# Kernel tuning notes

Hardware: AMD Instinct MI355X
Metric: run time of the kernel (lower is better)

Reference implementation:

```python
import jax, jax.numpy as jnp
import numpy as np
from jax import lax
from jax.scipy.special import ndtr

EV = 6           # even context kernel size
K = 3            # num_mixtures
GROUPS = 3       # grouped 1x1 convs (grps=3 for clrchs<3)
SCALE_MIN = 0.11 # lower bound on mixture std
LP = 257         # 257 CDF sampling points (8-bit Y/RGB path)


def _cdf_pts():
    # cdf_sampling_pts__Y_RGB from __init__
    pts = jnp.linspace(-127.5, 128.5, LP) / 255.0
    pts = pts.at[0].set(-147.5 / 255.0).at[-1].set(148.5 / 255.0)
    return pts.astype(jnp.float32)


def _conv(x, w, b, groups=1):
    y = lax.conv_general_dilated(
        x, w, window_strides=(1, 1), padding='VALID',
        dimension_numbers=('NCHW', 'OIHW', 'NCHW'),
        feature_group_count=groups)
    return y + b[None, :, None, None]


def _forward_float(y_condition, W0, b0, W1, b1, W2, b2):
    # replicate pad: paddd0_00_11 = (Ev//2-1, Ev//2, Ev//2-1, Ev//2)
    y = jnp.pad(y_condition, ((0, 0), (0, 0), (EV // 2 - 1, EV // 2), (EV // 2 - 1, EV // 2)), mode='edge')
    h = jax.nn.relu(_conv(y, W0, b0, groups=1))        # [B, 192, H, W]
    h = jax.nn.relu(_conv(h, W1, b1, groups=GROUPS))   # [B, 192, H, W]
    p = _conv(h, W2, b2, groups=GROUPS)                # [B, 9, H, W] GMM params
    B, _, H, W = p.shape
    p = p.reshape(B, 3, K, H, W)                       # param-major: mu / raw_scale / raw_weight
    mu, sr, wr = p[:, 0], p[:, 1], p[:, 2]             # each [B, K, H, W]
    scale = jnp.maximum(jnp.exp(sr), SCALE_MIN)
    wts = jax.nn.softmax(wr, axis=1)                   # mixture weights over K
    t = _cdf_pts()                                     # [LP]
    z = (t - mu[..., None]) / scale[..., None]         # [B, K, H, W, LP]
    cdf = jnp.einsum('bkhw,bkhwl->bhwl', wts, ndtr(z)) # mixture CDF, [B, H, W, LP]
    return jnp.clip(cdf, 0.0, 1.0 - 1e-6)


def setup_inputs() -> dict:
    key = jax.random.key(0)
    ks = jax.random.split(key, 4)
    return {
        'y_condition': jax.random.uniform(ks[0], (1, 1, 256, 256), jnp.float32),
        'W0': jax.random.normal(ks[1], (192, 1, EV, EV), jnp.float32) * 0.05,
        'b0': jnp.zeros((192,), jnp.float32),
        'W1': jax.random.normal(ks[2], (192, 64, 1, 1), jnp.float32) * 0.05,
        'b1': jnp.zeros((192,), jnp.float32),
        'W2': jax.random.normal(ks[3], (9, 64, 1, 1), jnp.float32) * 0.05,
        'b2': jnp.zeros((9,), jnp.float32),
    }


def reference(y_condition, W0, b0, W1, b1, W2, b2):
    cdf_f = _forward_float(y_condition, W0, b0, W1, b1, W2, b2)
    # _convert_to_int_and_normalize with needs_normalization=True
    new_max = jnp.float32(2 ** 16 - (LP - 1))
    cdf_i = jnp.round(cdf_f * new_max).astype(jnp.int16)
    cdf_i = cdf_i + jnp.arange(LP, dtype=jnp.int16)
    return cdf_i
```

## Files before the change

### kernel.cpp

```cpp
#include <hip/hip_runtime.h>
#include <math.h>

#define LPTS 257
#define NPIX 65536
#define PPB  32


__device__ __forceinline__ float xla_exp32(float x)
{
#pragma clang fp contract(off)
    x = fminf(x, 88.3762626647950f);
    x = fmaxf(x, -87.3365478515625f);
    const float m = floorf(fmaf(x, 1.44269504088896341f, 0.5f));
    float r = fmaf(m, -0.693359375f, x);
    r = fmaf(m, 2.12194440e-4f, r);
    const float r2 = r * r;
    float p = 1.9875691500e-4f;
    p = fmaf(p, r, 1.3981999507e-3f);
    p = fmaf(p, r, 8.3334519073e-3f);
    p = fmaf(p, r, 4.1665795894e-2f);
    p = fmaf(p, r, 1.6666665459e-1f);
    p = fmaf(p, r, 5.0000001201e-1f);
    float y = fmaf(p, r2, r) + 1.0f;
    const int e = (int)m;
    const float s = __int_as_float((e + 127) << 23);
    return y * s;
}

__device__ __forceinline__ float ieee_div(float n, float d)
{
    const float r0 = __builtin_amdgcn_rcpf(d);
    const float e  = fmaf(-d, r0, 1.0f);
    const float r1 = fmaf(e, r0, r0);
    const float q0 = n * r1;
    const float e1 = fmaf(-d, q0, n);
    const float q1 = fmaf(e1, r1, q0);
    const float e2 = fmaf(-d, q1, n);
    return fmaf(e2, r1, q1);
}

__device__ __forceinline__ float xla_erf32(float x)
{
#pragma clang fp contract(off)
    x = fminf(fmaxf(x, -4.0f), 4.0f);
    const float x2 = x * x;
    float pa = -2.72614225801306e-10f;
    pa = fmaf(pa, x2, 2.77068142495902e-08f);
    pa = fmaf(pa, x2, -2.10102402082508e-06f);
    pa = fmaf(pa, x2, -5.69250639462346e-05f);
    pa = fmaf(pa, x2, -7.34990630326855e-04f);
    pa = fmaf(pa, x2, -2.95459980854025e-03f);
    pa = fmaf(pa, x2, -1.60960333262415e-02f);
    float pb = -1.45660718464996e-05f;
    pb = fmaf(pb, x2, -2.13374055278905e-04f);
    pb = fmaf(pb, x2, -1.68282697438203e-03f);
    pb = fmaf(pb, x2, -7.37332916720468e-03f);
    pb = fmaf(pb, x2, -1.42647390514189e-02f);
    return ieee_div(x * pa, pb);
}

__device__ __forceinline__ float xla_erfc_ge1(float x)
{
#pragma clang fp contract(off)
    const float z = xla_exp32(-(x * x));
    const float q = 1.0f / x;
    const float y2 = q * q;
    float p;
    if (x < 2.0f) {
        p = 2.326819970068386e-02f;
        p = fmaf(p, y2, -1.387039388740657e-01f);
        p = fmaf(p, y2, 3.687424674597105e-01f);
        p = fmaf(p, y2, -5.824733027278666e-01f);
        p = fmaf(p, y2, 6.210004621745983e-01f);
        p = fmaf(p, y2, -4.944515323274145e-01f);
        p = fmaf(p, y2, 3.404879937665872e-01f);
        p = fmaf(p, y2, -2.741127028184656e-01f);
        p = fmaf(p, y2, 5.638259427386472e-01f);
    } else {
        p = -1.047766399936249e+01f;
        p = fmaf(p, y2, 1.297719955372516e+01f);
        p = fmaf(p, y2, -7.495518717768503e+00f);
        p = fmaf(p, y2, 2.921019019210786e+00f);
        p = fmaf(p, y2, -1.015265279202700e+00f);
        p = fmaf(p, y2, 4.218463358204948e-01f);
        p = fmaf(p, y2, -2.820767439740514e-01f);
        p = fmaf(p, y2, 5.641895067754075e-01f);
    }
    return z * q * p;
}

__device__ __forceinline__ void xla_ndtr3_y(
    float z0, float z1, float z2, float& o0, float& o1, float& o2)
{
#pragma clang fp contract(off)
    const float c = __uint_as_float(0x3f3504f3u);
    const float w0 = z0 * c, w1 = z1 * c, w2 = z2 * c;
    const float a0 = fabsf(w0), a1 = fabsf(w1), a2 = fabsf(w2);

    const float E0 = xla_erf32(w0);
    const float E1 = xla_erf32(w1);
    const float E2 = xla_erf32(w2);

    const float m0 = 1.0f - fabsf(E0);
    const float m1 = 1.0f - fabsf(E1);
    const float m2 = 1.0f - fabsf(E2);

    float y0 = (a0 < c) ? (1.0f + E0) : ((w0 > 0.0f) ? (2.0f - m0) : m0);
    float y1 = (a1 < c) ? (1.0f + E1) : ((w1 > 0.0f) ? (2.0f - m1) : m1);
    float y2 = (a2 < c) ? (1.0f + E2) : ((w2 > 0.0f) ? (2.0f - m2) : m2);

    const float amax = fmaxf(fmaxf(a0, a1), a2);
    if (__builtin_expect(__ballot(amax > 1.0f) != 0ull, 0)) {
        {
            const float ec = xla_erfc_ge1(a0);
            const float yc = (w0 > 0.0f) ? (2.0f - ec) : ec;
            y0 = (a0 > 1.0f) ? yc : y0;
        }
        {
            const float ec = xla_erfc_ge1(a1);
            const float yc = (w1 > 0.0f) ? (2.0f - ec) : ec;
            y1 = (a1 > 1.0f) ? yc : y1;
        }
        {
            const float ec = xla_erfc_ge1(a2);
            const float yc = (w2 > 0.0f) ? (2.0f - ec) : ec;
            y2 = (a2 > 1.0f) ? yc : y2;
        }
    }
    o0 = y0; o1 = y1; o2 = y2;
}

__device__ __forceinline__ float xla_ndtr32(float zf)
{
#pragma clang fp contract(off)
    const float c = __uint_as_float(0x3f3504f3u);
    const float w = zf * c;
    const float aw = fabsf(w);
    const float E = xla_erf32(w);
    const float e_mid = 1.0f - fabsf(E);
    float y = (aw < c) ? (1.0f + E)
                       : ((w > 0.0f) ? (2.0f - e_mid) : e_mid);
    if (__builtin_expect(__ballot(aw > 1.0f) != 0ull, 0)) {
        const float ec = xla_erfc_ge1(aw);
        const float yc = (w > 0.0f) ? (2.0f - ec) : ec;
        y = (aw > 1.0f) ? yc : y;
    }
    return 0.5f * y;
}

__device__ __forceinline__ int quantize(float cdf, int l)
{
    int r = (int)rintf(cdf * 65280.0f);
    r = r > 32767 ? 32767 : r;
    r = r < -32768 ? -32768 : r;
    return (int)((short)(r + l));
}

__global__ __launch_bounds__(256, 2) void entropy_params(
    const float* __restrict__ y,
    const float* __restrict__ W0, const float* __restrict__ b0,
    const float* __restrict__ W1, const float* __restrict__ b1,
    const float* __restrict__ W2, const float* __restrict__ b2,
    float* __restrict__ prm_g)
{
#pragma clang fp contract(off)
    __shared__ float tile[21][22];
    __shared__ __align__(16) float w0s[64 * 36];
    __shared__ __align__(16) float w1s[64 * 64];
    __shared__ __align__(16) float w2s[3 * 64];
    __shared__ __align__(16) float b0s[64];
    __shared__ __align__(16) float b1s[64];
    __shared__ float b2s[3];

    const int bx  = blockIdx.x & 15;
    const int by  = blockIdx.x >> 4;
    const int g   = blockIdx.y;
    const int tid = threadIdx.x;
    const int tx  = tid & 15;
    const int ty  = tid >> 4;

    {
        const float4* src = (const float4*)(W0 + g * 64 * 36);
        for (int i = tid; i < 576; i += 256) ((float4*)w0s)[i] = src[i];
    }
    {
        const float4* src = (const float4*)(W1 + g * 64 * 64);
        for (int i = tid; i < 1024; i += 256) ((float4*)w1s)[i] = src[i];
    }
    {
        const float4* src = (const float4*)(W2 + g * 3 * 64);
        if (tid < 48) ((float4*)w2s)[tid] = src[tid];
    }
    {
        const float4* s0 = (const float4*)(b0 + g * 64);
        const float4* s1 = (const float4*)(b1 + g * 64);
        if (tid < 16)      ((float4*)b0s)[tid]      = s0[tid];
        else if (tid < 32) ((float4*)b1s)[tid - 16] = s1[tid - 16];
        if (tid < 3) b2s[tid] = b2[3 * g + tid];
    }

    for (int idx = tid; idx < 21 * 21; idx += 256) {
        const int r = idx / 21;
        const int c = idx - r * 21;
        int gy = by * 16 - 2 + r; gy = gy < 0 ? 0 : (gy > 255 ? 255 : gy);
        int gx = bx * 16 - 2 + c; gx = gx < 0 ? 0 : (gx > 255 ? 255 : gx);
        tile[r][c] = y[gy * 256 + gx];
    }
    __syncthreads();

    float patch[36];
#pragma unroll
    for (int i = 0; i < 6; ++i)
#pragma unroll
        for (int j = 0; j < 6; ++j)
            patch[i * 6 + j] = tile[ty + i][tx + j];

    float h0[64];
#pragma unroll
    for (int c = 0; c < 64; ++c) {
        const float4* w4 = (const float4*)(w0s + c * 36);
        float acc = 0.0f;
#pragma unroll
        for (int q = 0; q < 9; ++q) {
            const float4 wv = w4[q];
            acc = fmaf(wv.x, patch[4 * q + 0], acc);
            acc = fmaf(wv.y, patch[4 * q + 1], acc);
            acc = fmaf(wv.z, patch[4 * q + 2], acc);
            acc = fmaf(wv.w, patch[4 * q + 3], acc);
        }
        acc = acc + b0s[c];
        h0[c] = fmaxf(acc, 0.0f);
    }

    float p0 = 0.0f, p1 = 0.0f, p2 = 0.0f;
#pragma unroll 4
    for (int c = 0; c < 64; ++c) {
        const float4* w4 = (const float4*)(w1s + c * 64);
        float acc = 0.0f;
#pragma unroll
        for (int q = 0; q < 16; ++q) {
            const float4 wv = w4[q];
            acc = fmaf(wv.x, h0[4 * q + 0], acc);
            acc = fmaf(wv.y, h0[4 * q + 1], acc);
            acc = fmaf(wv.z, h0[4 * q + 2], acc);
            acc = fmaf(wv.w, h0[4 * q + 3], acc);
        }
        acc = acc + b1s[c];
        acc = fmaxf(acc, 0.0f);
        p0 = fmaf(w2s[0 * 64 + c], acc, p0);
        p1 = fmaf(w2s[1 * 64 + c], acc, p1);
        p2 = fmaf(w2s[2 * 64 + c], acc, p2);
    }
    p0 = p0 + b2s[0];
    p1 = p1 + b2s[1];
    p2 = p2 + b2s[2];

    const int pix = (by * 16 + ty) * 256 + bx * 16 + tx;

    if (g == 0) {
        prm_g[0 * NPIX + pix] = p0;
        prm_g[1 * NPIX + pix] = p1;
        prm_g[2 * NPIX + pix] = p2;
    } else if (g == 1) {
        const float s0 = fmaxf(xla_exp32(p0), 0.11f);
        const float s1 = fmaxf(xla_exp32(p1), 0.11f);
        const float s2 = fmaxf(xla_exp32(p2), 0.11f);
        prm_g[3 * NPIX + pix] = s0;
        prm_g[4 * NPIX + pix] = s1;
        prm_g[5 * NPIX + pix] = s2;
        prm_g[6 * NPIX + pix] = 1.0f / s0;
        prm_g[7 * NPIX + pix] = 1.0f / s1;
        prm_g[8 * NPIX + pix] = 1.0f / s2;
    } else {
        const float m  = fmaxf(fmaxf(p0, p1), p2);
        const float e0 = xla_exp32(p0 - m);
        const float e1 = xla_exp32(p1 - m);
        const float e2 = xla_exp32(p2 - m);
        const float s  = (e0 + e1) + e2;
        prm_g[ 9 * NPIX + pix] = 0.5f * (e0 / s);
        prm_g[10 * NPIX + pix] = 0.5f * (e1 / s);
        prm_g[11 * NPIX + pix] = 0.5f * (e2 / s);
    }
}

__global__ __launch_bounds__(256) void entropy_cdf(
    const float* __restrict__ prm_g,
    int* __restrict__ out)
{
#pragma clang fp contract(off)
    __shared__ __align__(16) float prm[PPB][12];

    const int base = blockIdx.x * PPB;
    const int tid  = threadIdx.x;

    for (int i = tid; i < 12 * PPB; i += 256) {
        const int j = i >> 5;
        const int p = i & 31;
        prm[p][j] = prm_g[j * NPIX + base + p];
    }
    __syncthreads();

    const float CLIP = (float)(1.0 - 1e-6);

    {
        const int l = tid;
        const float t32 = (l == 0)
            ? (float)(-147.5 / 255.0)
            : (float)((((double)l) - 127.5) / 255.0);
#pragma unroll 4
        for (int p = 0; p < PPB; ++p) {
            const float4 v0 = *(const float4*)&prm[p][0];
            const float4 v1 = *(const float4*)&prm[p][4];
            const float4 v2 = *(const float4*)&prm[p][8];

            const float x0 = t32 - v0.x;
            const float x1 = t32 - v0.y;
            const float x2 = t32 - v0.z;
            const float qa = x0 * v1.z;
            const float qb = x1 * v1.w;
            const float qc = x2 * v2.x;
            const float ra = fmaf(-v0.w, qa, x0);
            const float rb = fmaf(-v1.x, qb, x1);
            const float rc = fmaf(-v1.y, qc, x2);
            const float z0 = fmaf(ra, v1.z, qa);
            const float z1 = fmaf(rb, v1.w, qb);
            const float z2 = fmaf(rc, v2.x, qc);

            float y0, y1, y2;
            xla_ndtr3_y(z0, z1, z2, y0, y1, y2);

            float cdf = fmaf(v2.w, y2, fmaf(v2.z, y1, v2.y * y0));
            cdf = fminf(fmaxf(cdf, 0.0f), CLIP);

            out[(size_t)(base + p) * LPTS + l] = quantize(cdf, l);
        }
    }

    if (tid < PPB) {
        const int p = tid;
        const float t32 = (float)(148.5 / 255.0);
        const float4 v0 = *(const float4*)&prm[p][0];
        const float4 v1 = *(const float4*)&prm[p][4];
        const float4 v2 = *(const float4*)&prm[p][8];

        const float x0 = t32 - v0.x;
        const float x1 = t32 - v0.y;
        const float x2 = t32 - v0.z;
        const float qa = x0 * v1.z;
        const float qb = x1 * v1.w;
        const float qc = x2 * v2.x;
        const float ra = fmaf(-v0.w, qa, x0);
        const float rb = fmaf(-v1.x, qb, x1);
        const float rc = fmaf(-v1.y, qc, x2);
        const float z0 = fmaf(ra, v1.z, qa);
        const float z1 = fmaf(rb, v1.w, qb);
        const float z2 = fmaf(rc, v2.x, qc);

        float y0, y1, y2;
        xla_ndtr3_y(z0, z1, z2, y0, y1, y2);

        float cdf = fmaf(v2.w, y2, fmaf(v2.z, y1, v2.y * y0));
        cdf = fminf(fmaxf(cdf, 0.0f), CLIP);

        out[(size_t)(base + p) * LPTS + 256] = quantize(cdf, 256);
    }
}

__global__ __launch_bounds__(256) void entropy_fused(
    const float* __restrict__ y,
    const float* __restrict__ W0, const float* __restrict__ b0,
    const float* __restrict__ W1, const float* __restrict__ b1,
    const float* __restrict__ W2, const float* __restrict__ b2,
    int* __restrict__ out)
{
#pragma clang fp contract(off)

    __shared__ float tile[21][22];
    __shared__ float prm[9][257];

    const int bx  = blockIdx.x & 15;
    const int by  = blockIdx.x >> 4;
    const int tid = threadIdx.x;
    const int tx  = tid & 15;
    const int ty  = tid >> 4;

    for (int idx = tid; idx < 21 * 21; idx += 256) {
        const int r = idx / 21;
        const int c = idx - r * 21;
        int gy = by * 16 - 2 + r; gy = gy < 0 ? 0 : (gy > 255 ? 255 : gy);
        int gx = bx * 16 - 2 + c; gx = gx < 0 ? 0 : (gx > 255 ? 255 : gx);
        tile[r][c] = y[gy * 256 + gx];
    }
    __syncthreads();

    float patch[36];
#pragma unroll
    for (int i = 0; i < 6; ++i)
#pragma unroll
        for (int j = 0; j < 6; ++j)
            patch[i * 6 + j] = tile[ty + i][tx + j];

    for (int g = 0; g < 3; ++g) {
        float h0[64];
#pragma unroll
        for (int c = 0; c < 64; ++c) {
            float acc = 0.0f;
            const float* w = W0 + (g * 64 + c) * 36;
#pragma unroll
            for (int k = 0; k < 36; ++k)
                acc = fmaf(w[k], patch[k], acc);
            acc = acc + b0[g * 64 + c];
            h0[c] = fmaxf(acc, 0.0f);
        }

        float p0 = 0.0f, p1 = 0.0f, p2 = 0.0f;
#pragma unroll 2
        for (int c = 0; c < 64; ++c) {
            float acc = 0.0f;
            const float* w = W1 + (g * 64 + c) * 64;
#pragma unroll
            for (int j = 0; j < 64; ++j)
                acc = fmaf(w[j], h0[j], acc);
            acc = acc + b1[g * 64 + c];
            acc = fmaxf(acc, 0.0f);
            p0 = fmaf(W2[(3 * g + 0) * 64 + c], acc, p0);
            p1 = fmaf(W2[(3 * g + 1) * 64 + c], acc, p1);
            p2 = fmaf(W2[(3 * g + 2) * 64 + c], acc, p2);
        }
        p0 = p0 + b2[3 * g + 0];
        p1 = p1 + b2[3 * g + 1];
        p2 = p2 + b2[3 * g + 2];

        if (g == 0) {
            prm[0][tid] = p0; prm[1][tid] = p1; prm[2][tid] = p2;
        } else if (g == 1) {
            prm[3][tid] = fmaxf(xla_exp32(p0), 0.11f);
            prm[4][tid] = fmaxf(xla_exp32(p1), 0.11f);
            prm[5][tid] = fmaxf(xla_exp32(p2), 0.11f);
        } else {
            const float m  = fmaxf(fmaxf(p0, p1), p2);
            const float e0 = xla_exp32(p0 - m);
            const float e1 = xla_exp32(p1 - m);
            const float e2 = xla_exp32(p2 - m);
            const float s  = (e0 + e1) + e2;
            prm[6][tid] = e0 / s;
            prm[7][tid] = e1 / s;
            prm[8][tid] = e2 / s;
        }
    }
    __syncthreads();

    const int rowbase = (by * 16) * 256 + bx * 16;
    const float CLIP = (float)(1.0 - 1e-6);

    {
        const int l = tid;
        const float t32 = (l == 0)
            ? (float)(-147.5 / 255.0)
            : (float)((((double)l) - 127.5) / 255.0);
        for (int p = 0; p < 256; ++p) {
            const float mu0 = prm[0][p], mu1 = prm[1][p], mu2 = prm[2][p];
            const float sc0 = prm[3][p], sc1 = prm[4][p], sc2 = prm[5][p];
            const float w0  = prm[6][p], w1  = prm[7][p], w2  = prm[8][p];

            const float n0 = xla_ndtr32((t32 - mu0) / sc0);
            const float n1 = xla_ndtr32((t32 - mu1) / sc1);
            const float n2 = xla_ndtr32((t32 - mu2) / sc2);

            float cdf = fmaf(w2, n2, fmaf(w1, n1, w0 * n0));
            cdf = fminf(fmaxf(cdf, 0.0f), CLIP);

            const int pix = rowbase + (p >> 4) * 256 + (p & 15);
            out[(size_t)pix * LPTS + l] = quantize(cdf, l);
        }
    }

    {
        const int p = tid;
        const float t32 = (float)(148.5 / 255.0);
        const float mu0 = prm[0][p], mu1 = prm[1][p], mu2 = prm[2][p];
        const float sc0 = prm[3][p], sc1 = prm[4][p], sc2 = prm[5][p];
        const float w0  = prm[6][p], w1  = prm[7][p], w2  = prm[8][p];

        const float n0 = xla_ndtr32((t32 - mu0) / sc0);
        const float n1 = xla_ndtr32((t32 - mu1) / sc1);
        const float n2 = xla_ndtr32((t32 - mu2) / sc2);

        float cdf = fmaf(w2, n2, fmaf(w1, n1, w0 * n0));
        cdf = fminf(fmaxf(cdf, 0.0f), CLIP);

        const int pix = rowbase + (p >> 4) * 256 + (p & 15);
        out[(size_t)pix * LPTS + 256] = quantize(cdf, 256);
    }
}

extern "C" void kernel_launch(void* const* d_in, const int* in_sizes, int n_in,
                              void* d_out, int out_size, void* d_ws, size_t ws_size,
                              hipStream_t stream)
{
    const float* y  = (const float*)d_in[0];
    const float* W0 = (const float*)d_in[1];
    const float* b0 = (const float*)d_in[2];
    const float* W1 = (const float*)d_in[3];
    const float* b1 = (const float*)d_in[4];
    const float* W2 = (const float*)d_in[5];
    const float* b2 = (const float*)d_in[6];

    int* out = (int*)d_out;

    const size_t need = (size_t)12 * NPIX * sizeof(float);
    if (d_ws != nullptr && ws_size >= need) {
        float* prm_g = (float*)d_ws;
        entropy_params<<<dim3(256, 3), dim3(256), 0, stream>>>(
            y, W0, b0, W1, b1, W2, b2, prm_g);
        entropy_cdf<<<dim3(NPIX / PPB), dim3(256), 0, stream>>>(prm_g, out);
    } else {
        entropy_fused<<<dim3(256), dim3(256), 0, stream>>>(
            y, W0, b0, W1, b1, W2, b2, out);
    }
}
```

Measured before the change: 171.3 us.

## Compute two pixels per thread in params kernel with transposed W1 outer-product

The params kernel now uses 128-thread blocks, with each thread handling two pixels eight rows apart. W1 is stored transposed in shared memory with a padded row stride, and W2 is stored transposed. The first-layer activation for each input channel is computed on the fly and scattered into 64 second-layer accumulators per pixel, which removes the h0 array. The aim is to reuse each shared-memory weight load across two pixels and cut LDS traffic per FMA. The cost is much higher register pressure: 128 accumulators plus two 36-element patches, with launch bounds set to 1. That may lower occupancy or cause spills.

```diff
diff --git a/kernel.cpp b/kernel.cpp
--- a/kernel.cpp
+++ b/kernel.cpp
@@ -156,7 +156,9 @@
     return (int)((short)(r + l));
 }
 
-__global__ __launch_bounds__(256, 2) void entropy_params(
+#define W1T_LD 68
+
+__global__ __launch_bounds__(128, 1) void entropy_params(
     const float* __restrict__ y,
     const float* __restrict__ W0, const float* __restrict__ b0,
     const float* __restrict__ W1, const float* __restrict__ b1,
@@ -166,8 +168,8 @@
 #pragma clang fp contract(off)
     __shared__ float tile[21][22];
     __shared__ __align__(16) float w0s[64 * 36];
-    __shared__ __align__(16) float w1s[64 * 64];
-    __shared__ __align__(16) float w2s[3 * 64];
+    __shared__ __align__(16) float w1t[64 * W1T_LD];
+    __shared__ __align__(16) float w2t[64 * 4];
     __shared__ __align__(16) float b0s[64];
     __shared__ __align__(16) float b1s[64];
     __shared__ float b2s[3];
@@ -181,15 +183,26 @@
 
     {
         const float4* src = (const float4*)(W0 + g * 64 * 36);
-        for (int i = tid; i < 576; i += 256) ((float4*)w0s)[i] = src[i];
+        for (int i = tid; i < 576; i += 128) ((float4*)w0s)[i] = src[i];
     }
     {
-        const float4* src = (const float4*)(W1 + g * 64 * 64);
-        for (int i = tid; i < 1024; i += 256) ((float4*)w1s)[i] = src[i];
-    }
-    {
-        const float4* src = (const float4*)(W2 + g * 3 * 64);
-        if (tid < 48) ((float4*)w2s)[tid] = src[tid];
+        const float4* src = (const float4*)(W1 + g * 4096);
+        for (int i4 = tid; i4 < 1024; i4 += 128) {
+            const float4 v = src[i4];
+            const int c2 = i4 >> 4;
+            const int c1 = (i4 << 2) & 63;
+            w1t[(c1 + 0) * W1T_LD + c2] = v.x;
+            w1t[(c1 + 1) * W1T_LD + c2] = v.y;
+            w1t[(c1 + 2) * W1T_LD + c2] = v.z;
+            w1t[(c1 + 3) * W1T_LD + c2] = v.w;
+        }
+    }
+    if (tid < 64) {
+        const int c2 = tid;
+        w2t[c2 * 4 + 0] = W2[(3 * g + 0) * 64 + c2];
+        w2t[c2 * 4 + 1] = W2[(3 * g + 1) * 64 + c2];
+        w2t[c2 * 4 + 2] = W2[(3 * g + 2) * 64 + c2];
+        w2t[c2 * 4 + 3] = 0.0f;
     }
     {
         const float4* s0 = (const float4*)(b0 + g * 64);
@@ -198,8 +211,7 @@
         else if (tid < 32) ((float4*)b1s)[tid - 16] = s1[tid - 16];
         if (tid < 3) b2s[tid] = b2[3 * g + tid];
     }
-
-    for (int idx = tid; idx < 21 * 21; idx += 256) {
+    for (int idx = tid; idx < 21 * 21; idx += 128) {
         const int r = idx / 21;
         const int c = idx - r * 21;
         int gy = by * 16 - 2 + r; gy = gy < 0 ? 0 : (gy > 255 ? 255 : gy);
@@ -208,78 +220,119 @@
     }
     __syncthreads();
 
-    float patch[36];
+    float pA[36], pB[36];
 #pragma unroll
     for (int i = 0; i < 6; ++i)
 #pragma unroll
-        for (int j = 0; j < 6; ++j)
-            patch[i * 6 + j] = tile[ty + i][tx + j];
-
-    float h0[64];
-#pragma unroll
-    for (int c = 0; c < 64; ++c) {
-        const float4* w4 = (const float4*)(w0s + c * 36);
-        float acc = 0.0f;
+        for (int j = 0; j < 6; ++j) {
+            pA[i * 6 + j] = tile[ty + i][tx + j];
+            pB[i * 6 + j] = tile[ty + 8 + i][tx + j];
+        }
+
+    float a2a[64], a2b[64];
+#pragma unroll
+    for (int j = 0; j < 64; ++j) { a2a[j] = 0.0f; a2b[j] = 0.0f; }
+
+    for (int c1 = 0; c1 < 64; ++c1) {
+        const float4* w4 = (const float4*)(w0s + c1 * 36);
+        float ha = 0.0f, hb = 0.0f;
 #pragma unroll
         for (int q = 0; q < 9; ++q) {
             const float4 wv = w4[q];
-            acc = fmaf(wv.x, patch[4 * q + 0], acc);
-            acc = fmaf(wv.y, patch[4 * q + 1], acc);
-            acc = fmaf(wv.z, patch[4 * q + 2], acc);
-            acc = fmaf(wv.w, patch[4 * q + 3], acc);
-        }
-        acc = acc + b0s[c];
-        h0[c] = fmaxf(acc, 0.0f);
-    }
-
-    float p0 = 0.0f, p1 = 0.0f, p2 = 0.0f;
-#pragma unroll 4
-    for (int c = 0; c < 64; ++c) {
-        const float4* w4 = (const float4*)(w1s + c * 64);
-        float acc = 0.0f;
-#pragma unroll
-        for (int q = 0; q < 16; ++q) {
-            const float4 wv = w4[q];
-            acc = fmaf(wv.x, h0[4 * q + 0], acc);
-            acc = fmaf(wv.y, h0[4 * q + 1], acc);
-            acc = fmaf(wv.z, h0[4 * q + 2], acc);
-            acc = fmaf(wv.w, h0[4 * q + 3], acc);
-        }
-        acc = acc + b1s[c];
-        acc = fmaxf(acc, 0.0f);
-        p0 = fmaf(w2s[0 * 64 + c], acc, p0);
-        p1 = fmaf(w2s[1 * 64 + c], acc, p1);
-        p2 = fmaf(w2s[2 * 64 + c], acc, p2);
-    }
-    p0 = p0 + b2s[0];
-    p1 = p1 + b2s[1];
-    p2 = p2 + b2s[2];
-
-    const int pix = (by * 16 + ty) * 256 + bx * 16 + tx;
+            ha = fmaf(wv.x, pA[4 * q + 0], ha);
+            ha = fmaf(wv.y, pA[4 * q + 1], ha);
+            ha = fmaf(wv.z, pA[4 * q + 2], ha);
+            ha = fmaf(wv.w, pA[4 * q + 3], ha);
+            hb = fmaf(wv.x, pB[4 * q + 0], hb);
+            hb = fmaf(wv.y, pB[4 * q + 1], hb);
+            hb = fmaf(wv.z, pB[4 * q + 2], hb);
+            hb = fmaf(wv.w, pB[4 * q + 3], hb);
+        }
+        ha = fmaxf(ha + b0s[c1], 0.0f);
+        hb = fmaxf(hb + b0s[c1], 0.0f);
+
+        const float4* w1r = (const float4*)(w1t + c1 * W1T_LD);
+#pragma unroll
+        for (int qq = 0; qq < 16; ++qq) {
+            const float4 wv = w1r[qq];
+            a2a[4 * qq + 0] = fmaf(wv.x, ha, a2a[4 * qq + 0]);
+            a2a[4 * qq + 1] = fmaf(wv.y, ha, a2a[4 * qq + 1]);
+            a2a[4 * qq + 2] = fmaf(wv.z, ha, a2a[4 * qq + 2]);
+            a2a[4 * qq + 3] = fmaf(wv.w, ha, a2a[4 * qq + 3]);
+            a2b[4 * qq + 0] = fmaf(wv.x, hb, a2b[4 * qq + 0]);
+            a2b[4 * qq + 1] = fmaf(wv.y, hb, a2b[4 * qq + 1]);
+            a2b[4 * qq + 2] = fmaf(wv.z, hb, a2b[4 * qq + 2]);
+            a2b[4 * qq + 3] = fmaf(wv.w, hb, a2b[4 * qq + 3]);
+        }
+    }
+
+    float p0a = 0.0f, p1a = 0.0f, p2a = 0.0f;
+    float p0b = 0.0f, p1b = 0.0f, p2b = 0.0f;
+#pragma unroll
+    for (int c2 = 0; c2 < 64; ++c2) {
+        const float h1a = fmaxf(a2a[c2] + b1s[c2], 0.0f);
+        const float h1b = fmaxf(a2b[c2] + b1s[c2], 0.0f);
+        const float4 wv = *(const float4*)(w2t + c2 * 4);
+        p0a = fmaf(wv.x, h1a, p0a);
+        p1a = fmaf(wv.y, h1a, p1a);
+        p2a = fmaf(wv.z, h1a, p2a);
+        p0b = fmaf(wv.x, h1b, p0b);
+        p1b = fmaf(wv.y, h1b, p1b);
+        p2b = fmaf(wv.z, h1b, p2b);
+    }
+    p0a += b2s[0]; p1a += b2s[1]; p2a += b2s[2];
+    p0b += b2s[0]; p1b += b2s[1]; p2b += b2s[2];
+
+    const int pixA = (by * 16 + ty) * 256 + bx * 16 + tx;
+    const int pixB = pixA + 8 * 256;
 
     if (g == 0) {
-        prm_g[0 * NPIX + pix] = p0;
-        prm_g[1 * NPIX + pix] = p1;
-        prm_g[2 * NPIX + pix] = p2;
+        prm_g[0 * NPIX + pixA] = p0a;
+        prm_g[1 * NPIX + pixA] = p1a;
+        prm_g[2 * NPIX + pixA] = p2a;
+        prm_g[0 * NPIX + pixB] = p0b;
+        prm_g[1 * NPIX + pixB] = p1b;
+        prm_g[2 * NPIX + pixB] = p2b;
     } else if (g == 1) {
-        const float s0 = fmaxf(xla_exp32(p0), 0.11f);
-        const float s1 = fmaxf(xla_exp32(p1), 0.11f);
-        const float s2 = fmaxf(xla_exp32(p2), 0.11f);
-        prm_g[3 * NPIX + pix] = s0;
-        prm_g[4 * NPIX + pix] = s1;
-        prm_g[5 * NPIX + pix] = s2;
-        prm_g[6 * NPIX + pix] = 1.0f / s0;
-        prm_g[7 * NPIX + pix] = 1.0f / s1;
-        prm_g[8 * NPIX + pix] = 1.0f / s2;
+        const float s0a = fmaxf(xla_exp32(p0a), 0.11f);
+        const float s1a = fmaxf(xla_exp32(p1a), 0.11f);
+        const float s2a = fmaxf(xla_exp32(p2a), 0.11f);
+        const float s0b = fmaxf(xla_exp32(p0b), 0.11f);
+        const float s1b = fmaxf(xla_exp32(p1b), 0.11f);
+        const float s2b = fmaxf(xla_exp32(p2b), 0.11f);
+        prm_g[3 * NPIX + pixA] = s0a;
+        prm_g[4 * NPIX + pixA] = s1a;
+        prm_g[5 * NPIX + pixA] = s2a;
+        prm_g[6 * NPIX + pixA] = 1.0f / s0a;
+        prm_g[7 * NPIX + pixA] = 1.0f / s1a;
+        prm_g[8 * NPIX + pixA] = 1.0f / s2a;
+        prm_g[3 * NPIX + pixB] = s0b;
+        prm_g[4 * NPIX + pixB] = s1b;
+        prm_g[5 * NPIX + pixB] = s2b;
+        prm_g[6 * NPIX + pixB] = 1.0f / s0b;
+        prm_g[7 * NPIX + pixB] = 1.0f / s1b;
+        prm_g[8 * NPIX + pixB] = 1.0f / s2b;
     } else {
-        const float m  = fmaxf(fmaxf(p0, p1), p2);
-        const float e0 = xla_exp32(p0 - m);
-        const float e1 = xla_exp32(p1 - m);
-        const float e2 = xla_exp32(p2 - m);
-        const float s  = (e0 + e1) + e2;
-        prm_g[ 9 * NPIX + pix] = 0.5f * (e0 / s);
-        prm_g[10 * NPIX + pix] = 0.5f * (e1 / s);
-        prm_g[11 * NPIX + pix] = 0.5f * (e2 / s);
+        {
+            const float m  = fmaxf(fmaxf(p0a, p1a), p2a);
+            const float e0 = xla_exp32(p0a - m);
+            const float e1 = xla_exp32(p1a - m);
+            const float e2 = xla_exp32(p2a - m);
+            const float s  = (e0 + e1) + e2;
+            prm_g[ 9 * NPIX + pixA] = 0.5f * (e0 / s);
+            prm_g[10 * NPIX + pixA] = 0.5f * (e1 / s);
+            prm_g[11 * NPIX + pixA] = 0.5f * (e2 / s);
+        }
+        {
+            const float m  = fmaxf(fmaxf(p0b, p1b), p2b);
+            const float e0 = xla_exp32(p0b - m);
+            const float e1 = xla_exp32(p1b - m);
+            const float e2 = xla_exp32(p2b - m);
+            const float s  = (e0 + e1) + e2;
+            prm_g[ 9 * NPIX + pixB] = 0.5f * (e0 / s);
+            prm_g[10 * NPIX + pixB] = 0.5f * (e1 / s);
+            prm_g[11 * NPIX + pixB] = 0.5f * (e2 / s);
+        }
     }
 }
 
@@ -511,7 +564,7 @@
     const size_t need = (size_t)12 * NPIX * sizeof(float);
     if (d_ws != nullptr && ws_size >= need) {
         float* prm_g = (float*)d_ws;
-        entropy_params<<<dim3(256, 3), dim3(256), 0, stream>>>(
+        entropy_params<<<dim3(256, 3), dim3(128), 0, stream>>>(
             y, W0, b0, W1, b1, W2, b2, prm_g);
         entropy_cdf<<<dim3(NPIX / PPB), dim3(256), 0, stream>>>(prm_g, out);
     } else {
```

New measurement: 168.1 us. No clear change (-1.9%).

## Fuse conv0 into conv1 via outer-product accumulation with transposed W1

Applied to the files above, without the earlier changes.

Restructures the first two conv layers so each conv0 channel output is computed and immediately scattered into 64 conv1 accumulators, using a transposed, padded W1 layout in shared memory. This removes the need to hold all 64 h0 values live and then re-read them per output channel. W2 is also stored transposed as float4 per input channel. Launch bounds drop to one block per SM, which permits more registers but may reduce occupancy. The fused loop changes the FMA summation order for conv1, which could alter rounding slightly.

```diff
diff --git a/kernel.cpp b/kernel.cpp
--- a/kernel.cpp
+++ b/kernel.cpp
@@ -4,6 +4,7 @@
 #define LPTS 257
 #define NPIX 65536
 #define PPB  32
+#define W1T_LD 68
 
 
 __device__ __forceinline__ float xla_exp32(float x)
@@ -156,7 +157,7 @@
     return (int)((short)(r + l));
 }
 
-__global__ __launch_bounds__(256, 2) void entropy_params(
+__global__ __launch_bounds__(256, 1) void entropy_params(
     const float* __restrict__ y,
     const float* __restrict__ W0, const float* __restrict__ b0,
     const float* __restrict__ W1, const float* __restrict__ b1,
@@ -166,8 +167,8 @@
 #pragma clang fp contract(off)
     __shared__ float tile[21][22];
     __shared__ __align__(16) float w0s[64 * 36];
-    __shared__ __align__(16) float w1s[64 * 64];
-    __shared__ __align__(16) float w2s[3 * 64];
+    __shared__ __align__(16) float w1t[64 * W1T_LD];
+    __shared__ __align__(16) float w2t[64 * 4];
     __shared__ __align__(16) float b0s[64];
     __shared__ __align__(16) float b1s[64];
     __shared__ float b2s[3];
@@ -184,12 +185,23 @@
         for (int i = tid; i < 576; i += 256) ((float4*)w0s)[i] = src[i];
     }
     {
-        const float4* src = (const float4*)(W1 + g * 64 * 64);
-        for (int i = tid; i < 1024; i += 256) ((float4*)w1s)[i] = src[i];
-    }
-    {
-        const float4* src = (const float4*)(W2 + g * 3 * 64);
-        if (tid < 48) ((float4*)w2s)[tid] = src[tid];
+        const float4* src = (const float4*)(W1 + g * 4096);
+        for (int i4 = tid; i4 < 1024; i4 += 256) {
+            const float4 v = src[i4];
+            const int c2 = i4 >> 4;
+            const int c1 = (i4 << 2) & 63;
+            w1t[(c1 + 0) * W1T_LD + c2] = v.x;
+            w1t[(c1 + 1) * W1T_LD + c2] = v.y;
+            w1t[(c1 + 2) * W1T_LD + c2] = v.z;
+            w1t[(c1 + 3) * W1T_LD + c2] = v.w;
+        }
+    }
+    if (tid < 64) {
+        const int c2 = tid;
+        w2t[c2 * 4 + 0] = W2[(3 * g + 0) * 64 + c2];
+        w2t[c2 * 4 + 1] = W2[(3 * g + 1) * 64 + c2];
+        w2t[c2 * 4 + 2] = W2[(3 * g + 2) * 64 + c2];
+        w2t[c2 * 4 + 3] = 0.0f;
     }
     {
         const float4* s0 = (const float4*)(b0 + g * 64);
@@ -198,7 +210,6 @@
         else if (tid < 32) ((float4*)b1s)[tid - 16] = s1[tid - 16];
         if (tid < 3) b2s[tid] = b2[3 * g + tid];
     }
-
     for (int idx = tid; idx < 21 * 21; idx += 256) {
         const int r = idx / 21;
         const int c = idx - r * 21;
@@ -215,45 +226,45 @@
         for (int j = 0; j < 6; ++j)
             patch[i * 6 + j] = tile[ty + i][tx + j];
 
-    float h0[64];
-#pragma unroll
-    for (int c = 0; c < 64; ++c) {
-        const float4* w4 = (const float4*)(w0s + c * 36);
-        float acc = 0.0f;
+    float acc2[64];
+#pragma unroll
+    for (int j = 0; j < 64; ++j) acc2[j] = 0.0f;
+
+#pragma unroll 2
+    for (int c1 = 0; c1 < 64; ++c1) {
+        const float4* w4 = (const float4*)(w0s + c1 * 36);
+        float h = 0.0f;
 #pragma unroll
         for (int q = 0; q < 9; ++q) {
             const float4 wv = w4[q];
-            acc = fmaf(wv.x, patch[4 * q + 0], acc);
-            acc = fmaf(wv.y, patch[4 * q + 1], acc);
-            acc = fmaf(wv.z, patch[4 * q + 2], acc);
-            acc = fmaf(wv.w, patch[4 * q + 3], acc);
-        }
-        acc = acc + b0s[c];
-        h0[c] = fmaxf(acc, 0.0f);
+            h = fmaf(wv.x, patch[4 * q + 0], h);
+            h = fmaf(wv.y, patch[4 * q + 1], h);
+            h = fmaf(wv.z, patch[4 * q + 2], h);
+            h = fmaf(wv.w, patch[4 * q + 3], h);
+        }
+        h = fmaxf(h + b0s[c1], 0.0f);
+
+        const float4* w1r = (const float4*)(w1t + c1 * W1T_LD);
+#pragma unroll
+        for (int qq = 0; qq < 16; ++qq) {
+            const float4 wv = w1r[qq];
+            acc2[4 * qq + 0] = fmaf(wv.x, h, acc2[4 * qq + 0]);
+            acc2[4 * qq + 1] = fmaf(wv.y, h, acc2[4 * qq + 1]);
+            acc2[4 * qq + 2] = fmaf(wv.z, h, acc2[4 * qq + 2]);
+            acc2[4 * qq + 3] = fmaf(wv.w, h, acc2[4 * qq + 3]);
+        }
     }
 
     float p0 = 0.0f, p1 = 0.0f, p2 = 0.0f;
-#pragma unroll 4
-    for (int c = 0; c < 64; ++c) {
-        const float4* w4 = (const float4*)(w1s + c * 64);
-        float acc = 0.0f;
-#pragma unroll
-        for (int q = 0; q < 16; ++q) {
-            const float4 wv = w4[q];
-            acc = fmaf(wv.x, h0[4 * q + 0], acc);
-            acc = fmaf(wv.y, h0[4 * q + 1], acc);
-            acc = fmaf(wv.z, h0[4 * q + 2], acc);
-            acc = fmaf(wv.w, h0[4 * q + 3], acc);
-        }
-        acc = acc + b1s[c];
-        acc = fmaxf(acc, 0.0f);
-        p0 = fmaf(w2s[0 * 64 + c], acc, p0);
-        p1 = fmaf(w2s[1 * 64 + c], acc, p1);
-        p2 = fmaf(w2s[2 * 64 + c], acc, p2);
-    }
-    p0 = p0 + b2s[0];
-    p1 = p1 + b2s[1];
-    p2 = p2 + b2s[2];
+#pragma unroll
+    for (int c2 = 0; c2 < 64; ++c2) {
+        const float h1 = fmaxf(acc2[c2] + b1s[c2], 0.0f);
+        const float4 wv = *(const float4*)(w2t + c2 * 4);
+        p0 = fmaf(wv.x, h1, p0);
+        p1 = fmaf(wv.y, h1, p1);
+        p2 = fmaf(wv.z, h1, p2);
+    }
+    p0 += b2s[0]; p1 += b2s[1]; p2 += b2s[2];
 
     const int pix = (by * 16 + ty) * 256 + bx * 16 + tx;
 
```

New measurement: 175.1 us. 2.2% more time.
